# Kernel tuning notes

Hardware: AMD Instinct MI355X
Metric: run time of the kernel (lower is better)

Reference implementation:

```python
import jax, jax.numpy as jnp
import numpy as np

EPS = 1e-5


def setup_inputs() -> dict:
    key = jax.random.key(0)
    ks = jax.random.split(key, 8)
    g, p, d, h, w = 32, 64, 512, 24, 8
    hw = h * w
    return {
        "gal_fea": jax.random.normal(ks[0], (g, d, h, w), dtype=jnp.float32),
        "prob_fea": jax.random.normal(ks[1], (p, d, h, w), dtype=jnp.float32),
        "bn_weight": jnp.ones((1,), jnp.float32),
        "bn_bias": jnp.zeros((1,), jnp.float32),
        "bn_mean": jax.random.normal(ks[2], (1,), jnp.float32) * 0.1,
        "bn_var": jax.random.uniform(ks[3], (1,), jnp.float32, 0.5, 1.5),
        "fc_weight": jax.random.normal(ks[4], (1, 2 * hw), jnp.float32) * 0.05,
        "fc_bias": jnp.zeros((1,), jnp.float32),
        "lbn_weight": jnp.ones((1,), jnp.float32),
        "lbn_bias": jnp.zeros((1,), jnp.float32),
        "lbn_mean": jax.random.normal(ks[5], (1,), jnp.float32) * 0.1,
        "lbn_var": jax.random.uniform(ks[6], (1,), jnp.float32, 0.5, 1.5),
    }


def reference(gal_fea, prob_fea, bn_weight, bn_bias, bn_mean, bn_var,
              fc_weight, fc_bias, lbn_weight, lbn_bias, lbn_mean, lbn_var):
    g, d, h, w = gal_fea.shape
    p = prob_fea.shape[0]
    hw = h * w
    # 1x1 conv with probe pixels as kernels == batched correlation (QK^T style)
    gal = gal_fea.reshape(g, d, hw)                                  # [g, d, hw_x]
    ker = jnp.transpose(prob_fea, (0, 2, 3, 1)).reshape(p, hw, d)    # [p, hw_y, d]
    s = jnp.einsum('gdx,pyd->gpyx', gal, ker)                        # [g, p, hw_y, hw_x]
    # dual-axis max pooling, then concat: [g, p, 2*hw]
    score = jnp.concatenate([s.max(axis=2), s.max(axis=3)], axis=-1)
    # BatchNorm1d(1) in eval mode: scalar affine with running stats
    score = (score - bn_mean) * (bn_weight / jnp.sqrt(bn_var + EPS)) + bn_bias
    # fc: Linear(2*hw, 1)
    score = score.reshape(g * p, 2 * hw) @ fc_weight[0] + fc_bias[0]  # [g*p]
    score = score.reshape(g, p)
    # logit BatchNorm1d(1), eval mode
    score = (score - lbn_mean) * (lbn_weight / jnp.sqrt(lbn_var + EPS)) + lbn_bias
    return jax.nn.sigmoid(score / 10.0)
```

## Files before the change

### kernel.cpp

```cpp
#include <hip/hip_runtime.h>
#include <hip/hip_bf16.h>
#include <cstdint>
#include <cstddef>

#define NG 32
#define NP 64
#define ND 512
#define HW 192
#define KS 32
#define EPSV 1e-5f

typedef _Float16 half8 __attribute__((ext_vector_type(8)));
typedef float floatx4 __attribute__((ext_vector_type(4)));
typedef float floatx16 __attribute__((ext_vector_type(16)));

__global__ __launch_bounds__(256) void prep_frag(const float* __restrict__ gal,
                                                 const float* __restrict__ prob,
                                                 _Float16* __restrict__ galT4,
                                                 _Float16* __restrict__ probT4) {
  __shared__ float lds[16 * 192];
  const int z = blockIdx.x;
  const int ks = blockIdx.y;
  const float* src;
  _Float16* dst;
  if (z < NP) {
    src = prob + (size_t)z * ND * HW;
    dst = probT4 + (size_t)z * 98304;
  } else {
    src = gal + (size_t)(z - NP) * ND * HW;
    dst = galT4 + (size_t)(z - NP) * 98304;
  }
  src += (size_t)ks * 16 * HW;
  dst += (size_t)ks * 3072;
  const int t = threadIdx.x;
#pragma unroll
  for (int i = 0; i < 12; ++i) lds[i * 256 + t] = src[i * 256 + t];
  __syncthreads();
#pragma unroll
  for (int r = 0; r < 2; ++r) {
    const int h = r * 256 + t;
    if (h < 384) {
      const int rb = h >> 6, hi = (h >> 5) & 1, l31 = h & 31;
      half8 v;
#pragma unroll
      for (int j = 0; j < 8; ++j) v[j] = (_Float16)lds[(hi * 8 + j) * 192 + rb * 32 + l31];
      *(half8*)(dst + (size_t)h * 8) = v;
    }
  }
}

__global__ __launch_bounds__(256, 2) void qaconv_main(
    const _Float16* __restrict__ galT4, const _Float16* __restrict__ probT4,
    const float* __restrict__ bn_w, const float* __restrict__ bn_b,
    const float* __restrict__ bn_m, const float* __restrict__ bn_v,
    const float* __restrict__ fc_w, const float* __restrict__ fc_b,
    const float* __restrict__ lbn_w, const float* __restrict__ lbn_b,
    const float* __restrict__ lbn_m, const float* __restrict__ lbn_v,
    float* __restrict__ out) {
  __shared__ float colp[2][HW];
  __shared__ float rowpart[2][HW];
  __shared__ float wsum[4];

  const int bid = blockIdx.x;
  const int g = bid >> 6, p = bid & 63;

  const int t = threadIdx.x;
  const int lane = t & 63, wid = t >> 6;
  const int wr = wid & 1;
  const int wc = wid >> 1;
  const int l31 = lane & 31, hi = lane >> 5;

  const _Float16* pA = probT4 + (size_t)p * 98304 + wr * 1536 + lane * 8;
  const _Float16* pB = galT4 + (size_t)g * 98304 + wc * 1536 + lane * 8;

  floatx16 acc[3][3];
#pragma unroll
  for (int ii = 0; ii < 3; ++ii)
#pragma unroll
    for (int jj = 0; jj < 3; ++jj) acc[ii][jj] = (floatx16)0.f;

#define LOADF(AF, BF, ks_)                                   \
  {                                                          \
    const _Float16* a_ = pA + (size_t)(ks_)*3072;            \
    const _Float16* b_ = pB + (size_t)(ks_)*3072;            \
    AF[0] = *(const half8*)(a_);                             \
    AF[1] = *(const half8*)(a_ + 512);                       \
    AF[2] = *(const half8*)(a_ + 1024);                      \
    BF[0] = *(const half8*)(b_);                             \
    BF[1] = *(const half8*)(b_ + 512);                       \
    BF[2] = *(const half8*)(b_ + 1024);                      \
  }

#define MFMAS(AF, BF)                                                            \
  {                                                                              \
    __builtin_amdgcn_s_setprio(1);                                               \
    _Pragma("unroll") for (int ii = 0; ii < 3; ++ii)                             \
        _Pragma("unroll") for (int jj = 0; jj < 3; ++jj)                         \
            acc[ii][jj] = __builtin_amdgcn_mfma_f32_32x32x16_f16(AF[ii], BF[jj], \
                                                                 acc[ii][jj], 0, 0, 0); \
    __builtin_amdgcn_s_setprio(0);                                               \
  }

  half8 af0[3], bf0[3], af1[3], bf1[3];
  LOADF(af0, bf0, 0)
  LOADF(af1, bf1, 1)
  for (int ks = 0; ks < KS; ks += 2) {
    const int n0 = (ks + 2 < KS) ? ks + 2 : 30;
    const int n1 = (ks + 3 < KS) ? ks + 3 : 31;
    MFMAS(af0, bf0)
    LOADF(af0, bf0, n0)
    MFMAS(af1, bf1)
    LOADF(af1, bf1, n1)
  }

#pragma unroll
  for (int fb = 0; fb < 3; ++fb) {
    float v = -3.4e38f;
#pragma unroll
    for (int fa = 0; fa < 3; ++fa)
#pragma unroll
      for (int e = 0; e < 16; ++e) v = fmaxf(v, acc[fa][fb][e]);
    v = fmaxf(v, __shfl_xor(v, 32));
    if (lane < 32) colp[wr][wc * 96 + fb * 32 + lane] = v;
  }
#pragma unroll
  for (int fa = 0; fa < 3; ++fa)
#pragma unroll
    for (int e = 0; e < 16; ++e) {
      float rv = fmaxf(fmaxf(acc[fa][0][e], acc[fa][1][e]), acc[fa][2][e]);
      rv = fmaxf(rv, __shfl_xor(rv, 1));
      rv = fmaxf(rv, __shfl_xor(rv, 2));
      rv = fmaxf(rv, __shfl_xor(rv, 4));
      rv = fmaxf(rv, __shfl_xor(rv, 8));
      rv = fmaxf(rv, __shfl_xor(rv, 16));
      if (l31 == 0) {
        const int Y = wr * 96 + fa * 32 + (e & 3) + 8 * (e >> 2) + 4 * hi;
        rowpart[wc][Y] = rv;
      }
    }
  __syncthreads();

  float partial = 0.f;
  if (t < HW) {
    const float rmax = fmaxf(rowpart[0][t], rowpart[1][t]);
    const float cmax = fmaxf(colp[0][t], colp[1][t]);
    const float scale = bn_w[0] / sqrtf(bn_v[0] + EPSV);
    const float bm = bn_m[0], bb = bn_b[0];
    partial = ((cmax - bm) * scale + bb) * fc_w[t] +
              ((rmax - bm) * scale + bb) * fc_w[HW + t];
  }
#pragma unroll
  for (int off = 1; off < 64; off <<= 1) partial += __shfl_xor(partial, off);
  if (lane == 0) wsum[wid] = partial;
  __syncthreads();
  if (t == 0) {
    const float sum = fc_b[0] + wsum[0] + wsum[1] + wsum[2] + wsum[3];
    const float logit = (sum - lbn_m[0]) * (lbn_w[0] / sqrtf(lbn_v[0] + EPSV)) + lbn_b[0];
    out[bid] = 1.f / (1.f + expf(-logit * 0.1f));
  }
#undef LOADF
#undef MFMAS
}

__global__ __launch_bounds__(256) void qaconv_naive(
    const float* __restrict__ gal, const float* __restrict__ prob,
    const float* __restrict__ bn_w, const float* __restrict__ bn_b,
    const float* __restrict__ bn_m, const float* __restrict__ bn_v,
    const float* __restrict__ fc_w, const float* __restrict__ fc_b,
    const float* __restrict__ lbn_w, const float* __restrict__ lbn_b,
    const float* __restrict__ lbn_m, const float* __restrict__ lbn_v,
    float* __restrict__ out) {
  __shared__ float prow[ND];
  __shared__ float rowmaxs[HW];
  __shared__ float colmaxs[HW];
  __shared__ float red[4];
  const int bid = blockIdx.x;
  const int g = bid >> 6, p = bid & 63;
  const int t = threadIdx.x, lane = t & 63, wid = t >> 6;
  const float* gp = gal + (size_t)g * ND * HW;
  const float* pp = prob + (size_t)p * ND * HW;
  float colmax = -3.4e38f;
  for (int y = 0; y < HW; ++y) {
    for (int k = t; k < ND; k += 256) prow[k] = pp[(size_t)k * HW + y];
    __syncthreads();
    float sv = -3.4e38f;
    if (t < HW) {
      sv = 0.f;
      for (int k = 0; k < ND; ++k) sv = fmaf(prow[k], gp[(size_t)k * HW + t], sv);
      colmax = fmaxf(colmax, sv);
    }
    float m = sv;
#pragma unroll
    for (int off = 1; off < 64; off <<= 1) m = fmaxf(m, __shfl_xor(m, off));
    if (lane == 0) red[wid] = m;
    __syncthreads();
    if (t == 0) rowmaxs[y] = fmaxf(fmaxf(red[0], red[1]), fmaxf(red[2], red[3]));
    __syncthreads();
  }
  if (t < HW) colmaxs[t] = colmax;
  __syncthreads();
  float partial = 0.f;
  for (int j = t; j < 2 * HW; j += 256) {
    const float v = (j < HW) ? colmaxs[j] : rowmaxs[j - HW];
    const float sc = (v - bn_m[0]) * (bn_w[0] / sqrtf(bn_v[0] + EPSV)) + bn_b[0];
    partial += sc * fc_w[j];
  }
#pragma unroll
  for (int off = 1; off < 64; off <<= 1) partial += __shfl_xor(partial, off);
  if (lane == 0) red[wid] = partial;
  __syncthreads();
  if (t == 0) {
    const float sum = fc_b[0] + red[0] + red[1] + red[2] + red[3];
    const float logit = (sum - lbn_m[0]) * (lbn_w[0] / sqrtf(lbn_v[0] + EPSV)) + lbn_b[0];
    out[bid] = 1.f / (1.f + expf(-logit * 0.1f));
  }
}

extern "C" void kernel_launch(void* const* d_in, const int* in_sizes, int n_in,
                              void* d_out, int out_size, void* d_ws, size_t ws_size,
                              hipStream_t stream) {
  const float* gal = (const float*)d_in[0];
  const float* prob = (const float*)d_in[1];
  const float* bn_w = (const float*)d_in[2];
  const float* bn_b = (const float*)d_in[3];
  const float* bn_m = (const float*)d_in[4];
  const float* bn_v = (const float*)d_in[5];
  const float* fc_w = (const float*)d_in[6];
  const float* fc_b = (const float*)d_in[7];
  const float* lbn_w = (const float*)d_in[8];
  const float* lbn_b = (const float*)d_in[9];
  const float* lbn_m = (const float*)d_in[10];
  const float* lbn_v = (const float*)d_in[11];
  float* out = (float*)d_out;

  const size_t probT4_elems = (size_t)NP * 98304;
  const size_t galT4_elems = (size_t)NG * 98304;
  const size_t ws_needed = (probT4_elems + galT4_elems) * sizeof(_Float16);
  if (ws_size >= ws_needed) {
    _Float16* probT4 = (_Float16*)d_ws;
    _Float16* galT4 = probT4 + probT4_elems;
    prep_frag<<<dim3(NP + NG, KS), dim3(256), 0, stream>>>(gal, prob, galT4, probT4);
    qaconv_main<<<dim3(NG * NP), dim3(256), 0, stream>>>(
        galT4, probT4, bn_w, bn_b, bn_m, bn_v, fc_w, fc_b, lbn_w, lbn_b, lbn_m, lbn_v, out);
  } else {
    qaconv_naive<<<dim3(NG * NP), dim3(256), 0, stream>>>(
        gal, prob, bn_w, bn_b, bn_m, bn_v, fc_w, fc_b, lbn_w, lbn_b, lbn_m, lbn_v, out);
  }
}
```

Measured before the change: 109.2 us.

## Stage MFMA fragments through LDS with async global_load_lds triple buffering

Result: slower. 146.4 us (+34.1%).

```diff
diff --git a/kernel.cpp b/kernel.cpp
--- a/kernel.cpp
+++ b/kernel.cpp
@@ -49,6 +49,12 @@
   }
 }
 
+__device__ __forceinline__ void g2l16(const void* g, void* l) {
+  __builtin_amdgcn_global_load_lds(
+      (const __attribute__((address_space(1))) void*)g,
+      (__attribute__((address_space(3))) void*)l, 16, 0, 0);
+}
+
 __global__ __launch_bounds__(256, 2) void qaconv_main(
     const _Float16* __restrict__ galT4, const _Float16* __restrict__ probT4,
     const float* __restrict__ bn_w, const float* __restrict__ bn_b,
@@ -57,6 +63,7 @@
     const float* __restrict__ lbn_w, const float* __restrict__ lbn_b,
     const float* __restrict__ lbn_m, const float* __restrict__ lbn_v,
     float* __restrict__ out) {
+  __shared__ __align__(16) char tiles[4][3][6144];
   __shared__ float colp[2][HW];
   __shared__ float rowpart[2][HW];
   __shared__ float wsum[4];
@@ -72,6 +79,7 @@
 
   const _Float16* pA = probT4 + (size_t)p * 98304 + wr * 1536 + lane * 8;
   const _Float16* pB = galT4 + (size_t)g * 98304 + wc * 1536 + lane * 8;
+  char* myT = tiles[wid][0];
 
   floatx16 acc[3][3];
 #pragma unroll
@@ -79,39 +87,55 @@
 #pragma unroll
     for (int jj = 0; jj < 3; ++jj) acc[ii][jj] = (floatx16)0.f;
 
-#define LOADF(AF, BF, ks_)                                   \
-  {                                                          \
-    const _Float16* a_ = pA + (size_t)(ks_)*3072;            \
-    const _Float16* b_ = pB + (size_t)(ks_)*3072;            \
-    AF[0] = *(const half8*)(a_);                             \
-    AF[1] = *(const half8*)(a_ + 512);                       \
-    AF[2] = *(const half8*)(a_ + 1024);                      \
-    BF[0] = *(const half8*)(b_);                             \
-    BF[1] = *(const half8*)(b_ + 512);                       \
-    BF[2] = *(const half8*)(b_ + 1024);                      \
-  }
-
-#define MFMAS(AF, BF)                                                            \
-  {                                                                              \
-    __builtin_amdgcn_s_setprio(1);                                               \
-    _Pragma("unroll") for (int ii = 0; ii < 3; ++ii)                             \
-        _Pragma("unroll") for (int jj = 0; jj < 3; ++jj)                         \
-            acc[ii][jj] = __builtin_amdgcn_mfma_f32_32x32x16_f16(AF[ii], BF[jj], \
-                                                                 acc[ii][jj], 0, 0, 0); \
-    __builtin_amdgcn_s_setprio(0);                                               \
-  }
-
-  half8 af0[3], bf0[3], af1[3], bf1[3];
-  LOADF(af0, bf0, 0)
-  LOADF(af1, bf1, 1)
-  for (int ks = 0; ks < KS; ks += 2) {
-    const int n0 = (ks + 2 < KS) ? ks + 2 : 30;
-    const int n1 = (ks + 3 < KS) ? ks + 3 : 31;
-    MFMAS(af0, bf0)
-    LOADF(af0, bf0, n0)
-    MFMAS(af1, bf1)
-    LOADF(af1, bf1, n1)
-  }
+#define STAGE(sa_, sb_, off_)                 \
+  {                                           \
+    char* d_ = myT + (off_);                  \
+    g2l16((sa_), d_);                         \
+    g2l16((sa_) + 512, d_ + 1024);            \
+    g2l16((sa_) + 1024, d_ + 2048);           \
+    g2l16((sb_), d_ + 3072);                  \
+    g2l16((sb_) + 512, d_ + 4096);            \
+    g2l16((sb_) + 1024, d_ + 5120);           \
+  }
+
+  STAGE(pA, pB, 0)
+  STAGE(pA + 3072, pB + 3072, 6144)
+  const _Float16* sA = pA + 2 * 3072;
+  const _Float16* sB = pB + 2 * 3072;
+  int stOff = 12288;
+  int rdOff = 0;
+
+  for (int ks = 0; ks < KS; ++ks) {
+    if (ks < KS - 2) {
+      STAGE(sA, sB, stOff)
+      sA += 3072;
+      sB += 3072;
+      stOff = (stOff == 12288) ? 0 : stOff + 6144;
+      asm volatile("s_waitcnt vmcnt(12)" ::: "memory");
+    } else if (ks == KS - 2) {
+      asm volatile("s_waitcnt vmcnt(6)" ::: "memory");
+    } else {
+      asm volatile("s_waitcnt vmcnt(0)" ::: "memory");
+    }
+    const char* bA = myT + rdOff;
+    const char* bB = bA + 3072;
+    half8 af[3], bf[3];
+#pragma unroll
+    for (int f = 0; f < 3; ++f) {
+      af[f] = *(const half8*)(bA + f * 1024 + lane * 16);
+      bf[f] = *(const half8*)(bB + f * 1024 + lane * 16);
+    }
+    __builtin_amdgcn_s_setprio(1);
+#pragma unroll
+    for (int ii = 0; ii < 3; ++ii)
+#pragma unroll
+      for (int jj = 0; jj < 3; ++jj)
+        acc[ii][jj] =
+            __builtin_amdgcn_mfma_f32_32x32x16_f16(af[ii], bf[jj], acc[ii][jj], 0, 0, 0);
+    __builtin_amdgcn_s_setprio(0);
+    rdOff = (rdOff == 12288) ? 0 : rdOff + 6144;
+  }
+#undef STAGE
 
 #pragma unroll
   for (int fb = 0; fb < 3; ++fb) {
@@ -158,8 +182,6 @@
     const float logit = (sum - lbn_m[0]) * (lbn_w[0] / sqrtf(lbn_v[0] + EPSV)) + lbn_b[0];
     out[bid] = 1.f / (1.f + expf(-logit * 0.1f));
   }
-#undef LOADF
-#undef MFMAS
 }
 
 __global__ __launch_bounds__(256) void qaconv_naive(
```

## Stage MFMA operand tiles through LDS with async global-to-LDS loads

Applied to the files above, without the earlier changes.

After: 132.5 us. 21.3% more time.

```diff
diff --git a/kernel.cpp b/kernel.cpp
--- a/kernel.cpp
+++ b/kernel.cpp
@@ -49,6 +49,12 @@
   }
 }
 
+__device__ __forceinline__ void g2l16(const void* g, void* l) {
+  __builtin_amdgcn_global_load_lds(
+      (const __attribute__((address_space(1))) void*)g,
+      (__attribute__((address_space(3))) void*)l, 16, 0, 0);
+}
+
 __global__ __launch_bounds__(256, 2) void qaconv_main(
     const _Float16* __restrict__ galT4, const _Float16* __restrict__ probT4,
     const float* __restrict__ bn_w, const float* __restrict__ bn_b,
@@ -57,6 +63,7 @@
     const float* __restrict__ lbn_w, const float* __restrict__ lbn_b,
     const float* __restrict__ lbn_m, const float* __restrict__ lbn_v,
     float* __restrict__ out) {
+  __shared__ __align__(16) char tiles[4][12288];
   __shared__ float colp[2][HW];
   __shared__ float rowpart[2][HW];
   __shared__ float wsum[4];
@@ -70,8 +77,10 @@
   const int wc = wid >> 1;
   const int l31 = lane & 31, hi = lane >> 5;
 
-  const _Float16* pA = probT4 + (size_t)p * 98304 + wr * 1536 + lane * 8;
-  const _Float16* pB = galT4 + (size_t)g * 98304 + wc * 1536 + lane * 8;
+  const _Float16* srcA = probT4 + (size_t)p * 98304 + (wid & 1) * 1536 + lane * 8;
+  const _Float16* srcB = galT4 + (size_t)g * 98304 + (wid & 1) * 1536 + lane * 8;
+  const _Float16* mySrc = (wid < 2) ? srcA : srcB;
+  const int myDst = (wid >> 1) * 6144 + (wid & 1) * 3072;
 
   floatx16 acc[3][3];
 #pragma unroll
@@ -79,39 +88,50 @@
 #pragma unroll
     for (int jj = 0; jj < 3; ++jj) acc[ii][jj] = (floatx16)0.f;
 
-#define LOADF(AF, BF, ks_)                                   \
-  {                                                          \
-    const _Float16* a_ = pA + (size_t)(ks_)*3072;            \
-    const _Float16* b_ = pB + (size_t)(ks_)*3072;            \
-    AF[0] = *(const half8*)(a_);                             \
-    AF[1] = *(const half8*)(a_ + 512);                       \
-    AF[2] = *(const half8*)(a_ + 1024);                      \
-    BF[0] = *(const half8*)(b_);                             \
-    BF[1] = *(const half8*)(b_ + 512);                       \
-    BF[2] = *(const half8*)(b_ + 1024);                      \
-  }
-
-#define MFMAS(AF, BF)                                                            \
+#define STAGE(ks_, buf_)                                        \
+  {                                                             \
+    char* d_ = tiles[buf_] + myDst;                             \
+    const _Float16* s_ = mySrc + (size_t)(ks_)*3072;            \
+    g2l16(s_, d_);                                              \
+    g2l16(s_ + 512, d_ + 1024);                                 \
+    g2l16(s_ + 1024, d_ + 2048);                                \
+  }
+
+#define COMPUTE(buf_)                                                            \
   {                                                                              \
+    const char* bA = tiles[buf_];                                                \
+    const char* bB = bA + 6144;                                                  \
+    half8 af[3], bf[3];                                                          \
+    _Pragma("unroll") for (int f = 0; f < 3; ++f) {                              \
+      af[f] = *(const half8*)(bA + (wr * 3 + f) * 1024 + lane * 16);             \
+      bf[f] = *(const half8*)(bB + (wc * 3 + f) * 1024 + lane * 16);             \
+    }                                                                            \
     __builtin_amdgcn_s_setprio(1);                                               \
     _Pragma("unroll") for (int ii = 0; ii < 3; ++ii)                             \
         _Pragma("unroll") for (int jj = 0; jj < 3; ++jj)                         \
-            acc[ii][jj] = __builtin_amdgcn_mfma_f32_32x32x16_f16(AF[ii], BF[jj], \
+            acc[ii][jj] = __builtin_amdgcn_mfma_f32_32x32x16_f16(af[ii], bf[jj], \
                                                                  acc[ii][jj], 0, 0, 0); \
     __builtin_amdgcn_s_setprio(0);                                               \
   }
 
-  half8 af0[3], bf0[3], af1[3], bf1[3];
-  LOADF(af0, bf0, 0)
-  LOADF(af1, bf1, 1)
-  for (int ks = 0; ks < KS; ks += 2) {
-    const int n0 = (ks + 2 < KS) ? ks + 2 : 30;
-    const int n1 = (ks + 3 < KS) ? ks + 3 : 31;
-    MFMAS(af0, bf0)
-    LOADF(af0, bf0, n0)
-    MFMAS(af1, bf1)
-    LOADF(af1, bf1, n1)
-  }
+  STAGE(0, 0)
+  STAGE(1, 1)
+
+#pragma unroll 2
+  for (int kt = 0; kt < KS - 2; ++kt) {
+    STAGE(kt + 2, (kt + 2) & 3)
+    asm volatile("s_waitcnt vmcnt(6)" ::: "memory");
+    __builtin_amdgcn_s_barrier();
+    COMPUTE(kt & 3)
+  }
+  asm volatile("s_waitcnt vmcnt(3)" ::: "memory");
+  __builtin_amdgcn_s_barrier();
+  COMPUTE((KS - 2) & 3)
+  asm volatile("s_waitcnt vmcnt(0)" ::: "memory");
+  __builtin_amdgcn_s_barrier();
+  COMPUTE((KS - 1) & 3)
+#undef STAGE
+#undef COMPUTE
 
 #pragma unroll
   for (int fb = 0; fb < 3; ++fb) {
@@ -158,8 +178,6 @@
     const float logit = (sum - lbn_m[0]) * (lbn_w[0] / sqrtf(lbn_v[0] + EPSV)) + lbn_b[0];
     out[bid] = 1.f / (1.f + expf(-logit * 0.1f));
   }
-#undef LOADF
-#undef MFMAS
 }
 
 __global__ __launch_bounds__(256) void qaconv_naive(
```

## Stage operand tiles via async global-to-LDS triple buffering with 16x16x32 MFMA

Applied to the files above, without the earlier changes.

Result: slower. 113.3 us (+3.7%).

```diff
diff --git a/kernel.cpp b/kernel.cpp
--- a/kernel.cpp
+++ b/kernel.cpp
@@ -7,143 +7,188 @@
 #define NP 64
 #define ND 512
 #define HW 192
-#define KS 32
+#define KT16 16
 #define EPSV 1e-5f
 
 typedef _Float16 half8 __attribute__((ext_vector_type(8)));
 typedef float floatx4 __attribute__((ext_vector_type(4)));
-typedef float floatx16 __attribute__((ext_vector_type(16)));
-
-__global__ __launch_bounds__(256) void prep_frag(const float* __restrict__ gal,
-                                                 const float* __restrict__ prob,
-                                                 _Float16* __restrict__ galT4,
-                                                 _Float16* __restrict__ probT4) {
-  __shared__ float lds[16 * 192];
+
+__global__ __launch_bounds__(256) void prep_frag5(const float* __restrict__ gal,
+                                                  const float* __restrict__ prob,
+                                                  _Float16* __restrict__ galT5,
+                                                  _Float16* __restrict__ probT5) {
+  __shared__ float lds[32 * 192];
   const int z = blockIdx.x;
-  const int ks = blockIdx.y;
+  const int kt = blockIdx.y;
   const float* src;
   _Float16* dst;
   if (z < NP) {
     src = prob + (size_t)z * ND * HW;
-    dst = probT4 + (size_t)z * 98304;
+    dst = probT5 + (size_t)z * 98304;
   } else {
     src = gal + (size_t)(z - NP) * ND * HW;
-    dst = galT4 + (size_t)(z - NP) * 98304;
-  }
-  src += (size_t)ks * 16 * HW;
-  dst += (size_t)ks * 3072;
+    dst = galT5 + (size_t)(z - NP) * 98304;
+  }
+  src += (size_t)kt * 32 * HW;
+  dst += (size_t)kt * 6144;
   const int t = threadIdx.x;
 #pragma unroll
-  for (int i = 0; i < 12; ++i) lds[i * 256 + t] = src[i * 256 + t];
-  __syncthreads();
-#pragma unroll
-  for (int r = 0; r < 2; ++r) {
+  for (int i = 0; i < 24; ++i) lds[i * 256 + t] = src[i * 256 + t];
+  __syncthreads();
+#pragma unroll
+  for (int r = 0; r < 3; ++r) {
     const int h = r * 256 + t;
-    if (h < 384) {
-      const int rb = h >> 6, hi = (h >> 5) & 1, l31 = h & 31;
-      half8 v;
-#pragma unroll
-      for (int j = 0; j < 8; ++j) v[j] = (_Float16)lds[(hi * 8 + j) * 192 + rb * 32 + l31];
-      *(half8*)(dst + (size_t)h * 8) = v;
-    }
-  }
-}
-
-__global__ __launch_bounds__(256, 2) void qaconv_main(
-    const _Float16* __restrict__ galT4, const _Float16* __restrict__ probT4,
+    const int rb = h >> 6, l = h & 63;
+    const int row = rb * 16 + (l & 15), dk = (l >> 4) * 8;
+    half8 v;
+#pragma unroll
+    for (int j = 0; j < 8; ++j) v[j] = (_Float16)lds[(dk + j) * 192 + row];
+    *(half8*)(dst + (size_t)h * 8) = v;
+  }
+}
+
+__device__ __forceinline__ void g2l16(const void* g, void* l) {
+  __builtin_amdgcn_global_load_lds(
+      (const __attribute__((address_space(1))) void*)g,
+      (__attribute__((address_space(3))) void*)l, 16, 0, 0);
+}
+
+__global__ __launch_bounds__(512, 4) void qaconv_main(
+    const _Float16* __restrict__ galT5, const _Float16* __restrict__ probT5,
     const float* __restrict__ bn_w, const float* __restrict__ bn_b,
     const float* __restrict__ bn_m, const float* __restrict__ bn_v,
     const float* __restrict__ fc_w, const float* __restrict__ fc_b,
     const float* __restrict__ lbn_w, const float* __restrict__ lbn_b,
     const float* __restrict__ lbn_m, const float* __restrict__ lbn_v,
     float* __restrict__ out) {
-  __shared__ float colp[2][HW];
+  __shared__ __align__(16) char tiles[3][24576];
+  __shared__ float colp[4][HW];
   __shared__ float rowpart[2][HW];
-  __shared__ float wsum[4];
+  __shared__ float wsum[8];
 
   const int bid = blockIdx.x;
   const int g = bid >> 6, p = bid & 63;
 
   const int t = threadIdx.x;
   const int lane = t & 63, wid = t >> 6;
-  const int wr = wid & 1;
-  const int wc = wid >> 1;
-  const int l31 = lane & 31, hi = lane >> 5;
-
-  const _Float16* pA = probT4 + (size_t)p * 98304 + wr * 1536 + lane * 8;
-  const _Float16* pB = galT4 + (size_t)g * 98304 + wc * 1536 + lane * 8;
-
-  floatx16 acc[3][3];
+  const int wr = wid & 3;
+  const int wc = wid >> 2;
+  const int l15 = lane & 15, lhi = lane >> 4;
+
+  const _Float16* pAt = probT5 + (size_t)p * 98304 + lane * 8;
+  const _Float16* pBt = galT5 + (size_t)g * 98304 + lane * 8;
+
+  floatx4 acc[3][6];
 #pragma unroll
   for (int ii = 0; ii < 3; ++ii)
 #pragma unroll
-    for (int jj = 0; jj < 3; ++jj) acc[ii][jj] = (floatx16)0.f;
-
-#define LOADF(AF, BF, ks_)                                   \
+    for (int jj = 0; jj < 6; ++jj) acc[ii][jj] = (floatx4){0.f, 0.f, 0.f, 0.f};
+
+  half8 af[3], bf[6];
+
+#define STAGE(kt_, base_)                                                      \
+  {                                                                            \
+    _Pragma("unroll") for (int r_ = 0; r_ < 3; ++r_) {                         \
+      const int s0_ = r_ * 512 + wid * 64;                                     \
+      const _Float16* s_ = (s0_ < 768)                                         \
+                               ? (pAt + (size_t)(kt_)*6144 + (size_t)s0_ * 8)  \
+                               : (pBt + (size_t)(kt_)*6144 + (size_t)(s0_ - 768) * 8); \
+      g2l16(s_, (char*)(base_) + s0_ * 16);                                    \
+    }                                                                          \
+  }
+
+#define READ9(base_)                                                           \
+  {                                                                            \
+    const char* bA_ = (const char*)(base_);                                    \
+    const char* bB_ = (const char*)(base_) + 12288;                            \
+    af[0] = *(const half8*)(bA_ + (wr * 3 + 0) * 1024 + lane * 16);            \
+    af[1] = *(const half8*)(bA_ + (wr * 3 + 1) * 1024 + lane * 16);            \
+    af[2] = *(const half8*)(bA_ + (wr * 3 + 2) * 1024 + lane * 16);            \
+    bf[0] = *(const half8*)(bB_ + (wc * 6 + 0) * 1024 + lane * 16);            \
+    bf[1] = *(const half8*)(bB_ + (wc * 6 + 1) * 1024 + lane * 16);            \
+    bf[2] = *(const half8*)(bB_ + (wc * 6 + 2) * 1024 + lane * 16);            \
+    bf[3] = *(const half8*)(bB_ + (wc * 6 + 3) * 1024 + lane * 16);            \
+    bf[4] = *(const half8*)(bB_ + (wc * 6 + 4) * 1024 + lane * 16);            \
+    bf[5] = *(const half8*)(bB_ + (wc * 6 + 5) * 1024 + lane * 16);            \
+  }
+
+#define MFMA18()                                                               \
+  {                                                                            \
+    __builtin_amdgcn_s_setprio(1);                                             \
+    _Pragma("unroll") for (int ii = 0; ii < 3; ++ii)                           \
+        _Pragma("unroll") for (int jj = 0; jj < 6; ++jj)                       \
+            acc[ii][jj] = __builtin_amdgcn_mfma_f32_16x16x32_f16(af[ii], bf[jj],\
+                                                                 acc[ii][jj], 0, 0, 0); \
+    __builtin_amdgcn_s_setprio(0);                                             \
+  }
+
+#define SLOT(kt_, rdb_, stb_, doStage_, vmW_)                \
   {                                                          \
-    const _Float16* a_ = pA + (size_t)(ks_)*3072;            \
-    const _Float16* b_ = pB + (size_t)(ks_)*3072;            \
-    AF[0] = *(const half8*)(a_);                             \
-    AF[1] = *(const half8*)(a_ + 512);                       \
-    AF[2] = *(const half8*)(a_ + 1024);                      \
-    BF[0] = *(const half8*)(b_);                             \
-    BF[1] = *(const half8*)(b_ + 512);                       \
-    BF[2] = *(const half8*)(b_ + 1024);                      \
-  }
-
-#define MFMAS(AF, BF)                                                            \
-  {                                                                              \
-    __builtin_amdgcn_s_setprio(1);                                               \
-    _Pragma("unroll") for (int ii = 0; ii < 3; ++ii)                             \
-        _Pragma("unroll") for (int jj = 0; jj < 3; ++jj)                         \
-            acc[ii][jj] = __builtin_amdgcn_mfma_f32_32x32x16_f16(AF[ii], BF[jj], \
-                                                                 acc[ii][jj], 0, 0, 0); \
-    __builtin_amdgcn_s_setprio(0);                                               \
-  }
-
-  half8 af0[3], bf0[3], af1[3], bf1[3];
-  LOADF(af0, bf0, 0)
-  LOADF(af1, bf1, 1)
-  for (int ks = 0; ks < KS; ks += 2) {
-    const int n0 = (ks + 2 < KS) ? ks + 2 : 30;
-    const int n1 = (ks + 3 < KS) ? ks + 3 : 31;
-    MFMAS(af0, bf0)
-    LOADF(af0, bf0, n0)
-    MFMAS(af1, bf1)
-    LOADF(af1, bf1, n1)
-  }
-
-#pragma unroll
-  for (int fb = 0; fb < 3; ++fb) {
+    READ9(rdb_)                                              \
+    if (doStage_) STAGE((kt_) + 2, stb_)                     \
+    __builtin_amdgcn_sched_barrier(0);                       \
+    __builtin_amdgcn_s_barrier();                            \
+    asm volatile("s_waitcnt lgkmcnt(0)" ::: "memory");       \
+    __builtin_amdgcn_sched_barrier(0);                       \
+    MFMA18()                                                 \
+    asm volatile("s_waitcnt vmcnt(" #vmW_ ")" ::: "memory"); \
+    __builtin_amdgcn_s_barrier();                            \
+  }
+
+  STAGE(0, tiles[0])
+  STAGE(1, tiles[1])
+  asm volatile("s_waitcnt vmcnt(3)" ::: "memory");
+  __builtin_amdgcn_s_barrier();
+
+#pragma unroll 1
+  for (int m = 0; m < 4; ++m) {
+    SLOT(3 * m + 0, tiles[0], tiles[2], true, 3)
+    SLOT(3 * m + 1, tiles[1], tiles[0], true, 3)
+    SLOT(3 * m + 2, tiles[2], tiles[1], true, 3)
+  }
+  SLOT(12, tiles[0], tiles[2], true, 3)
+  SLOT(13, tiles[1], tiles[0], true, 3)
+  SLOT(14, tiles[2], tiles[1], false, 0)
+  READ9(tiles[0])
+  asm volatile("s_waitcnt lgkmcnt(0)" ::: "memory");
+  __builtin_amdgcn_sched_barrier(0);
+  MFMA18()
+#undef STAGE
+#undef READ9
+#undef MFMA18
+#undef SLOT
+
+#pragma unroll
+  for (int fc = 0; fc < 6; ++fc) {
     float v = -3.4e38f;
 #pragma unroll
-    for (int fa = 0; fa < 3; ++fa)
-#pragma unroll
-      for (int e = 0; e < 16; ++e) v = fmaxf(v, acc[fa][fb][e]);
+    for (int fr = 0; fr < 3; ++fr)
+#pragma unroll
+      for (int r = 0; r < 4; ++r) v = fmaxf(v, acc[fr][fc][r]);
+    v = fmaxf(v, __shfl_xor(v, 16));
     v = fmaxf(v, __shfl_xor(v, 32));
-    if (lane < 32) colp[wr][wc * 96 + fb * 32 + lane] = v;
-  }
-#pragma unroll
-  for (int fa = 0; fa < 3; ++fa)
-#pragma unroll
-    for (int e = 0; e < 16; ++e) {
-      float rv = fmaxf(fmaxf(acc[fa][0][e], acc[fa][1][e]), acc[fa][2][e]);
+    if (lane < 16) colp[wr][wc * 96 + fc * 16 + lane] = v;
+  }
+#pragma unroll
+  for (int fr = 0; fr < 3; ++fr)
+#pragma unroll
+    for (int r = 0; r < 4; ++r) {
+      float rv = acc[fr][0][r];
+#pragma unroll
+      for (int fc = 1; fc < 6; ++fc) rv = fmaxf(rv, acc[fr][fc][r]);
       rv = fmaxf(rv, __shfl_xor(rv, 1));
       rv = fmaxf(rv, __shfl_xor(rv, 2));
       rv = fmaxf(rv, __shfl_xor(rv, 4));
       rv = fmaxf(rv, __shfl_xor(rv, 8));
-      rv = fmaxf(rv, __shfl_xor(rv, 16));
-      if (l31 == 0) {
-        const int Y = wr * 96 + fa * 32 + (e & 3) + 8 * (e >> 2) + 4 * hi;
-        rowpart[wc][Y] = rv;
-      }
+      if (l15 == 0) rowpart[wc][wr * 48 + fr * 16 + lhi * 4 + r] = rv;
     }
   __syncthreads();
 
   float partial = 0.f;
   if (t < HW) {
     const float rmax = fmaxf(rowpart[0][t], rowpart[1][t]);
-    const float cmax = fmaxf(colp[0][t], colp[1][t]);
+    const float cmax =
+        fmaxf(fmaxf(colp[0][t], colp[1][t]), fmaxf(colp[2][t], colp[3][t]));
     const float scale = bn_w[0] / sqrtf(bn_v[0] + EPSV);
     const float bm = bn_m[0], bb = bn_b[0];
     partial = ((cmax - bm) * scale + bb) * fc_w[t] +
@@ -154,12 +199,12 @@
   if (lane == 0) wsum[wid] = partial;
   __syncthreads();
   if (t == 0) {
-    const float sum = fc_b[0] + wsum[0] + wsum[1] + wsum[2] + wsum[3];
+    float sum = fc_b[0];
+#pragma unroll
+    for (int w = 0; w < 8; ++w) sum += wsum[w];
     const float logit = (sum - lbn_m[0]) * (lbn_w[0] / sqrtf(lbn_v[0] + EPSV)) + lbn_b[0];
     out[bid] = 1.f / (1.f + expf(-logit * 0.1f));
   }
-#undef LOADF
-#undef MFMAS
 }
 
 __global__ __launch_bounds__(256) void qaconv_naive(
@@ -233,15 +278,15 @@
   const float* lbn_v = (const float*)d_in[11];
   float* out = (float*)d_out;
 
-  const size_t probT4_elems = (size_t)NP * 98304;
-  const size_t galT4_elems = (size_t)NG * 98304;
-  const size_t ws_needed = (probT4_elems + galT4_elems) * sizeof(_Float16);
+  const size_t probT5_elems = (size_t)NP * 98304;
+  const size_t galT5_elems = (size_t)NG * 98304;
+  const size_t ws_needed = (probT5_elems + galT5_elems) * sizeof(_Float16);
   if (ws_size >= ws_needed) {
-    _Float16* probT4 = (_Float16*)d_ws;
-    _Float16* galT4 = probT4 + probT4_elems;
-    prep_frag<<<dim3(NP + NG, KS), dim3(256), 0, stream>>>(gal, prob, galT4, probT4);
-    qaconv_main<<<dim3(NG * NP), dim3(256), 0, stream>>>(
-        galT4, probT4, bn_w, bn_b, bn_m, bn_v, fc_w, fc_b, lbn_w, lbn_b, lbn_m, lbn_v, out);
+    _Float16* probT5 = (_Float16*)d_ws;
+    _Float16* galT5 = probT5 + probT5_elems;
+    prep_frag5<<<dim3(NP + NG, KT16), dim3(256), 0, stream>>>(gal, prob, galT5, probT5);
+    qaconv_main<<<dim3(NG * NP), dim3(512), 0, stream>>>(
+        galT5, probT5, bn_w, bn_b, bn_m, bn_v, fc_w, fc_b, lbn_w, lbn_b, lbn_m, lbn_v, out);
   } else {
     qaconv_naive<<<dim3(NG * NP), dim3(256), 0, stream>>>(
         gal, prob, bn_w, bn_b, bn_m, bn_v, fc_w, fc_b, lbn_w, lbn_b, lbn_m, lbn_v, out);
```
